# Kernel optimization log

Measured on AMD Instinct MI355X. Metric: run time of the kernel, lower is better.

Reference implementation:

```python
import jax, jax.numpy as jnp
import numpy as np

BETA = 0.001  # init kwarg beta
S, K = 32768, 32  # segments x candidates-per-segment (uniform segments)


def setup_inputs() -> dict:
    key = jax.random.key(0)
    logits = jax.random.normal(key, (S * K,), dtype=jnp.float32)
    # cumulative segment offsets: [0, K, 2K, ..., S*K]  (uniform ragged structure)
    k_lens = jnp.arange(S + 1, dtype=jnp.int32) * K
    return {"logits": logits, "k_lens": k_lens}


def reference(logits, k_lens):
    # Static shapes derived from array shapes (uniform segments).
    n_seg = k_lens.shape[0] - 1              # S
    seg_len = logits.shape[0] // n_seg       # K
    seg = logits.reshape(n_seg, seg_len)     # [S, K]
    # torch.combinations(arange(K), 2) == upper-triangular index pairs (i < j)
    i_idx, j_idx = jnp.triu_indices(seg_len, k=1)  # each [P], P = K*(K-1)/2
    pos = seg[:, i_idx]                      # [S, P]
    neg = seg[:, j_idx]                      # [S, P]
    l2 = 0.5 * (pos * pos - neg * neg)
    # per-segment loss: -mean(logsigmoid(pos-neg) + beta*l2)
    loss = -jnp.mean(jax.nn.log_sigmoid(pos - neg) + BETA * l2, axis=1)  # [S]
    return loss  # reduction=None -> stacked per-segment losses
```

## Files before the change

kernel.cpp:

```cpp
#include <hip/hip_runtime.h>


constexpr int K = 32;

#if __has_builtin(__builtin_amdgcn_exp2f)
#define FAST_EXP2(x) __builtin_amdgcn_exp2f(x)
#else
#define FAST_EXP2(x) exp2f(x)
#endif
#if __has_builtin(__builtin_amdgcn_logf)
#define FAST_LOG2(x) __builtin_amdgcn_logf(x)
#else
#define FAST_LOG2(x) log2f(x)
#endif

#define XSTEP(M)                                                          \
    do {                                                                  \
        const float ep = __int_as_float(__builtin_amdgcn_ds_swizzle(      \
            __float_as_int(e), ((M) << 10) | 0x1f));                      \
        prod *= fmaf(ep, f, 1.0f);                                        \
    } while (0)

#define RSTEP(M)                                                          \
    r += __int_as_float(__builtin_amdgcn_ds_swizzle(                      \
        __float_as_int(r), ((M) << 10) | 0x1f))

__global__ __launch_bounds__(1024) void rmloss_kernel(
        const float* __restrict__ logits, float* __restrict__ out, int n_seg) {
    const int lane = threadIdx.x & 63;
    const int wave = blockIdx.x * 16 + (threadIdx.x >> 6);
    const int seg0 = wave * 2;
    if (seg0 >= n_seg) return;

    const long long gidx = (long long)wave * 64 + lane;
    float x = 0.0f;
    if (gidx < (long long)n_seg * K) x = logits[gidx];

    constexpr float LOG2E = 1.4426950408889634f;
    constexpr float LN2   = 0.6931471805599453f;
    const float y = x * LOG2E;
    const float e = FAST_EXP2(y);
    const float f = FAST_EXP2(-y);

    float acc, prod = 1.0f;
    XSTEP(1);  XSTEP(2);  XSTEP(3);  XSTEP(4);
    XSTEP(5);  XSTEP(6);  XSTEP(7);  XSTEP(8);
    acc = FAST_LOG2(prod); prod = 1.0f;
    XSTEP(9);  XSTEP(10); XSTEP(11); XSTEP(12);
    XSTEP(13); XSTEP(14); XSTEP(15); XSTEP(16);
    acc += FAST_LOG2(prod); prod = 1.0f;
    XSTEP(17); XSTEP(18); XSTEP(19); XSTEP(20);
    XSTEP(21); XSTEP(22); XSTEP(23); XSTEP(24);
    acc += FAST_LOG2(prod); prod = 1.0f;
    XSTEP(25); XSTEP(26); XSTEP(27); XSTEP(28);
    XSTEP(29); XSTEP(30); XSTEP(31);
    acc += FAST_LOG2(prod);

    const int   k = lane & 31;
    const float c = (float)(2 * k - 31);
    float r = fmaf(0.5f * LN2, acc, c * x * fmaf(0.0005f, x, 0.5f));

    RSTEP(16); RSTEP(8); RSTEP(4); RSTEP(2); RSTEP(1);

    if ((lane & 31) == 0) {
        const int seg = seg0 + (lane >> 5);
        if (seg < n_seg) out[seg] = r * (1.0f / 496.0f);
    }
}

extern "C" void kernel_launch(void* const* d_in, const int* in_sizes, int n_in,
                              void* d_out, int out_size, void* d_ws, size_t ws_size,
                              hipStream_t stream) {
    const float* logits = (const float*)d_in[0];
    const int n_seg = in_sizes[1] - 1;
    float* out = (float*)d_out;
    const int segs_per_block = 32;
    const int blocks = (n_seg + segs_per_block - 1) / segs_per_block;
    rmloss_kernel<<<blocks, 1024, 0, stream>>>(logits, out, n_seg);
}
```

Measured before the change: 58.10 us.

## Compute each segment's pairwise loss serially in a single thread

Replaces the wave-level scheme, where each lane held one logit and exchanged values with partners via ds_swizzle, with a one-thread-per-segment mapping. Each thread loads its 32 logits as float4s and walks the 496 unordered pairs directly, batching log2 over products of eight softplus factors, so the doubled ordered-pair work and the cross-lane shuffles and reductions go away. In exchange the grid shrinks to 512 wavefronts of serial dependent multiply chains. That risks poor latency hiding and low device occupancy, and the per-thread loads are strided rather than coalesced.

```diff
diff --git a/kernel.cpp b/kernel.cpp
--- a/kernel.cpp
+++ b/kernel.cpp
@@ -14,58 +14,45 @@
 #define FAST_LOG2(x) log2f(x)
 #endif
 
-#define XSTEP(M)                                                          \
-    do {                                                                  \
-        const float ep = __int_as_float(__builtin_amdgcn_ds_swizzle(      \
-            __float_as_int(e), ((M) << 10) | 0x1f));                      \
-        prod *= fmaf(ep, f, 1.0f);                                        \
-    } while (0)
+__global__ __launch_bounds__(64) void rmloss_kernel(
+        const float* __restrict__ logits, float* __restrict__ out, int n_seg) {
+    const int seg = blockIdx.x * 64 + threadIdx.x;
+    if (seg >= n_seg) return;
 
-#define RSTEP(M)                                                          \
-    r += __int_as_float(__builtin_amdgcn_ds_swizzle(                      \
-        __float_as_int(r), ((M) << 10) | 0x1f))
-
-__global__ __launch_bounds__(1024) void rmloss_kernel(
-        const float* __restrict__ logits, float* __restrict__ out, int n_seg) {
-    const int lane = threadIdx.x & 63;
-    const int wave = blockIdx.x * 16 + (threadIdx.x >> 6);
-    const int seg0 = wave * 2;
-    if (seg0 >= n_seg) return;
-
-    const long long gidx = (long long)wave * 64 + lane;
-    float x = 0.0f;
-    if (gidx < (long long)n_seg * K) x = logits[gidx];
+    const float4* p = reinterpret_cast<const float4*>(logits + (long long)seg * K);
+    float x[K];
+#pragma unroll
+    for (int q = 0; q < K / 4; ++q) {
+        const float4 v = p[q];
+        x[4 * q + 0] = v.x; x[4 * q + 1] = v.y;
+        x[4 * q + 2] = v.z; x[4 * q + 3] = v.w;
+    }
 
     constexpr float LOG2E = 1.4426950408889634f;
     constexpr float LN2   = 0.6931471805599453f;
-    const float y = x * LOG2E;
-    const float e = FAST_EXP2(y);
-    const float f = FAST_EXP2(-y);
 
-    float acc, prod = 1.0f;
-    XSTEP(1);  XSTEP(2);  XSTEP(3);  XSTEP(4);
-    XSTEP(5);  XSTEP(6);  XSTEP(7);  XSTEP(8);
-    acc = FAST_LOG2(prod); prod = 1.0f;
-    XSTEP(9);  XSTEP(10); XSTEP(11); XSTEP(12);
-    XSTEP(13); XSTEP(14); XSTEP(15); XSTEP(16);
-    acc += FAST_LOG2(prod); prod = 1.0f;
-    XSTEP(17); XSTEP(18); XSTEP(19); XSTEP(20);
-    XSTEP(21); XSTEP(22); XSTEP(23); XSTEP(24);
-    acc += FAST_LOG2(prod); prod = 1.0f;
-    XSTEP(25); XSTEP(26); XSTEP(27); XSTEP(28);
-    XSTEP(29); XSTEP(30); XSTEP(31);
-    acc += FAST_LOG2(prod);
+    float f[K];
+    float bsum = 0.0f;
+#pragma unroll
+    for (int k = 0; k < K; ++k) {
+        f[k] = FAST_EXP2(-x[k] * LOG2E);
+        bsum = fmaf((float)(31 - 2 * k) * x[k], x[k], bsum);
+    }
 
-    const int   k = lane & 31;
-    const float c = (float)(2 * k - 31);
-    float r = fmaf(0.5f * LN2, acc, c * x * fmaf(0.0005f, x, 0.5f));
+    float sp = 0.0f, prod = 1.0f;
+    int cnt = 0;
+#pragma unroll
+    for (int j = 1; j < K; ++j) {
+        const float ej = FAST_EXP2(x[j] * LOG2E);
+#pragma unroll
+        for (int i = 0; i < j; ++i) {
+            prod *= fmaf(ej, f[i], 1.0f);
+            if (++cnt == 8) { sp += FAST_LOG2(prod); prod = 1.0f; cnt = 0; }
+        }
+    }
+    sp += FAST_LOG2(prod);
 
-    RSTEP(16); RSTEP(8); RSTEP(4); RSTEP(2); RSTEP(1);
-
-    if ((lane & 31) == 0) {
-        const int seg = seg0 + (lane >> 5);
-        if (seg < n_seg) out[seg] = r * (1.0f / 496.0f);
-    }
+    out[seg] = (LN2 * sp - 0.0005f * bsum) * (1.0f / 496.0f);
 }
 
 extern "C" void kernel_launch(void* const* d_in, const int* in_sizes, int n_in,
@@ -74,7 +61,7 @@
     const float* logits = (const float*)d_in[0];
     const int n_seg = in_sizes[1] - 1;
     float* out = (float*)d_out;
-    const int segs_per_block = 32;
-    const int blocks = (n_seg + segs_per_block - 1) / segs_per_block;
-    rmloss_kernel<<<blocks, 1024, 0, stream>>>(logits, out, n_seg);
+    const int threads = 64;
+    const int blocks = (n_seg + threads - 1) / threads;
+    rmloss_kernel<<<blocks, threads, 0, stream>>>(logits, out, n_seg);
 }
```

Result: no change. 57.73 us (-0.6%).
